# Performance work log

Measured on AMD Instinct MI355X. Metric: run time of the kernel, lower is better.

The kernel has to match this reference:

```python
import jax, jax.numpy as jnp
import numpy as np

B, N = 16384, 2048  # batch, number of digits


def setup_inputs() -> dict:
    key = jax.random.key(0)
    k1, k2 = jax.random.split(key)
    a = jax.random.randint(k1, (B, N), 0, 10).astype(jnp.float32)
    b = jax.random.randint(k2, (B, N), 0, 10).astype(jnp.float32)
    # Fixed weights from RNNAdder.__init__
    w_ih = jnp.ones((2, 2), jnp.float32)                      # rnn.weight_ih_l0
    w_hh = jnp.array([[1.0, -1.0], [1.0, -1.0]], jnp.float32)  # rnn.weight_hh_l0
    b_ih = jnp.zeros((2,), jnp.float32)                       # rnn.bias_ih_l0
    b_hh = jnp.array([-9.0, -10.0], jnp.float32)              # rnn.bias_hh_l0
    w_carry = jnp.array([[1.0, -1.0]], jnp.float32)           # carry_out.weight
    return {"a": a, "b": b, "w_ih": w_ih, "w_hh": w_hh,
            "b_ih": b_ih, "b_hh": b_hh, "w_carry": w_carry}


def reference(a, b, w_ih, w_hh, b_ih, b_hh, w_carry):
    batch, n = a.shape
    # LSB-first digit streams (torch: stack then flip(1))
    a_r = a[:, ::-1]
    b_r = b[:, ::-1]
    x = jnp.stack([a_r, b_r], axis=2)          # (B, N, 2)
    xs = jnp.transpose(x, (1, 0, 2))            # (N, B, 2) time-major for scan

    h_init = jnp.zeros((batch, 2), a.dtype)

    def step(h, xt):
        # Elman RNN cell with relu nonlinearity (batch_first RNN unrolled)
        h_new = jax.nn.relu(xt @ w_ih.T + b_ih + h @ w_hh.T + b_hh)
        return h_new, h_new

    h_fin, h_seq = jax.lax.scan(step, h_init, xs)   # h_fin (B,2), h_seq (N,B,2)

    # carry_out linear (no bias): (N,B,2) @ (2,1) -> (N,B) -> (B,N)
    carry = jnp.moveaxis((h_seq @ w_carry.T)[..., 0], 0, 1)
    carry_prev = jnp.concatenate(
        [jnp.zeros((batch, 1), a.dtype), carry[:, :-1]], axis=1)

    s = a_r + b_r + carry_prev
    digits = jnp.round(s - 10.0 * carry)[:, ::-1].astype(jnp.int32)  # MSB-first
    final_carry = jnp.round(h_fin @ w_carry.T).astype(jnp.int32)     # (B,1)
    return jnp.concatenate([final_carry, digits], axis=1)            # (B, N+1)
```

## Files before the change

### kernel.cpp

```cpp
#include <hip/hip_runtime.h>


#define NDIG 2048
#define TPB 256
#define DPT 8

__global__ __launch_bounds__(TPB) void rnn_adder_kernel(
    const float* __restrict__ A, const float* __restrict__ B,
    int* __restrict__ out) {
  const int row = blockIdx.x;
  const int t = threadIdx.x;
  const int base = NDIG - (t + 1) * DPT;

  const float4* A4 = reinterpret_cast<const float4*>(A + (size_t)row * NDIG + base);
  const float4* B4 = reinterpret_cast<const float4*>(B + (size_t)row * NDIG + base);
  float4 a0 = A4[0], a1 = A4[1];
  float4 b0 = B4[0], b1 = B4[1];

  int s[DPT];
  s[0] = (int)a0.x + (int)b0.x;
  s[1] = (int)a0.y + (int)b0.y;
  s[2] = (int)a0.z + (int)b0.z;
  s[3] = (int)a0.w + (int)b0.w;
  s[4] = (int)a1.x + (int)b1.x;
  s[5] = (int)a1.y + (int)b1.y;
  s[6] = (int)a1.z + (int)b1.z;
  s[7] = (int)a1.w + (int)b1.w;

  int c0 = 0, c1 = 1;
#pragma unroll
  for (int k = DPT - 1; k >= 0; --k) {
    c0 = (s[k] + c0) >= 10;
    c1 = (s[k] + c1) >= 10;
  }

  __shared__ int sc[TPB];
  int cur = c0 | (c1 << 1);
  sc[t] = cur;
  __syncthreads();

#pragma unroll
  for (int off = 1; off < TPB; off <<= 1) {
    int prev = (t >= off) ? sc[t - off] : 2;
    __syncthreads();
    int p0 = prev & 1, p1 = (prev >> 1) & 1;
    cur = ((cur >> p0) & 1) | (((cur >> p1) & 1) << 1);
    sc[t] = cur;
    __syncthreads();
  }

  int cin = (t == 0) ? 0 : (sc[t - 1] & 1);

  int c = cin;
  int d[DPT];
#pragma unroll
  for (int k = DPT - 1; k >= 0; --k) {
    int v = s[k] + c;
    c = (v >= 10);
    d[k] = v - 10 * c;
  }

  int* orow = out + (size_t)row * (NDIG + 1);
#pragma unroll
  for (int k = 0; k < DPT; ++k) orow[1 + base + k] = d[k];
  if (t == TPB - 1) orow[0] = c;
}

extern "C" void kernel_launch(void* const* d_in, const int* in_sizes, int n_in,
                              void* d_out, int out_size, void* d_ws, size_t ws_size,
                              hipStream_t stream) {
  const float* A = (const float*)d_in[0];
  const float* B = (const float*)d_in[1];
  int* out = (int*)d_out;
  const int rows = in_sizes[0] / NDIG;
  rnn_adder_kernel<<<rows, TPB, 0, stream>>>(A, B, out);
}
```

Baseline: 74.94 us.

## Map one row per wavefront and use shuffle-based carry scan

Each 64-lane wavefront now handles a whole row with 32 digits per lane, and four rows share a block. The shared-memory carry-state scan with block barriers becomes a wave-level __shfl_up scan with no barriers. The comparison against 10 is rewritten as an add-and-shift bit trick, and output goes through nontemporal stores. The cost is much higher register pressure per lane, and the output stores become strided per lane, which may hurt coalescing.

Result: slower. 244.6 us (+226.3%).

```diff
diff --git a/kernel.cpp b/kernel.cpp
--- a/kernel.cpp
+++ b/kernel.cpp
@@ -3,67 +3,66 @@
 
 #define NDIG 2048
 #define TPB 256
-#define DPT 8
+#define DPT 32
+#define RPB 4
 
 __global__ __launch_bounds__(TPB) void rnn_adder_kernel(
     const float* __restrict__ A, const float* __restrict__ B,
     int* __restrict__ out) {
-  const int row = blockIdx.x;
-  const int t = threadIdx.x;
-  const int base = NDIG - (t + 1) * DPT;
+  const int wave = threadIdx.x >> 6;
+  const int lane = threadIdx.x & 63;
+  const int row = blockIdx.x * RPB + wave;
+  const int base = NDIG - (lane + 1) * DPT;
 
   const float4* A4 = reinterpret_cast<const float4*>(A + (size_t)row * NDIG + base);
   const float4* B4 = reinterpret_cast<const float4*>(B + (size_t)row * NDIG + base);
-  float4 a0 = A4[0], a1 = A4[1];
-  float4 b0 = B4[0], b1 = B4[1];
+
+  float4 av[DPT / 4], bv[DPT / 4];
+#pragma unroll
+  for (int q = 0; q < DPT / 4; ++q) av[q] = A4[q];
+#pragma unroll
+  for (int q = 0; q < DPT / 4; ++q) bv[q] = B4[q];
 
   int s[DPT];
-  s[0] = (int)a0.x + (int)b0.x;
-  s[1] = (int)a0.y + (int)b0.y;
-  s[2] = (int)a0.z + (int)b0.z;
-  s[3] = (int)a0.w + (int)b0.w;
-  s[4] = (int)a1.x + (int)b1.x;
-  s[5] = (int)a1.y + (int)b1.y;
-  s[6] = (int)a1.z + (int)b1.z;
-  s[7] = (int)a1.w + (int)b1.w;
+#pragma unroll
+  for (int q = 0; q < DPT / 4; ++q) {
+    s[4 * q + 0] = (int)(av[q].x + bv[q].x);
+    s[4 * q + 1] = (int)(av[q].y + bv[q].y);
+    s[4 * q + 2] = (int)(av[q].z + bv[q].z);
+    s[4 * q + 3] = (int)(av[q].w + bv[q].w);
+  }
 
   int c0 = 0, c1 = 1;
 #pragma unroll
   for (int k = DPT - 1; k >= 0; --k) {
-    c0 = (s[k] + c0) >= 10;
-    c1 = (s[k] + c1) >= 10;
+    c0 = ((s[k] + c0 + 22) >> 5) & 1;
+    c1 = ((s[k] + c1 + 22) >> 5) & 1;
   }
 
-  __shared__ int sc[TPB];
   int cur = c0 | (c1 << 1);
-  sc[t] = cur;
-  __syncthreads();
-
 #pragma unroll
-  for (int off = 1; off < TPB; off <<= 1) {
-    int prev = (t >= off) ? sc[t - off] : 2;
-    __syncthreads();
-    int p0 = prev & 1, p1 = (prev >> 1) & 1;
-    cur = ((cur >> p0) & 1) | (((cur >> p1) & 1) << 1);
-    sc[t] = cur;
-    __syncthreads();
+  for (int off = 1; off < 64; off <<= 1) {
+    int prev = __shfl_up(cur, off, 64);
+    prev = (lane >= off) ? prev : 2;
+    cur = ((cur >> (prev & 1)) & 1) | (((cur >> ((prev >> 1) & 1)) & 1) << 1);
   }
 
-  int cin = (t == 0) ? 0 : (sc[t - 1] & 1);
+  int pr = __shfl_up(cur, 1, 64);
+  int cin = (lane == 0) ? 0 : (pr & 1);
 
   int c = cin;
-  int d[DPT];
 #pragma unroll
   for (int k = DPT - 1; k >= 0; --k) {
     int v = s[k] + c;
-    c = (v >= 10);
-    d[k] = v - 10 * c;
+    c = ((v + 22) >> 5) & 1;
+    s[k] = v - 10 * c;
   }
 
   int* orow = out + (size_t)row * (NDIG + 1);
 #pragma unroll
-  for (int k = 0; k < DPT; ++k) orow[1 + base + k] = d[k];
-  if (t == TPB - 1) orow[0] = c;
+  for (int k = 0; k < DPT; ++k)
+    __builtin_nontemporal_store(s[k], orow + 1 + base + k);
+  if (lane == 63) __builtin_nontemporal_store(c, orow);
 }
 
 extern "C" void kernel_launch(void* const* d_in, const int* in_sizes, int n_in,
@@ -73,5 +72,5 @@
   const float* B = (const float*)d_in[1];
   int* out = (int*)d_out;
   const int rows = in_sizes[0] / NDIG;
-  rnn_adder_kernel<<<rows, TPB, 0, stream>>>(A, B, out);
+  rnn_adder_kernel<<<rows / RPB, TPB, 0, stream>>>(A, B, out);
 }
```
